# Kernel optimization log

Hardware: AMD Instinct MI355X
Metric: run time of the kernel (lower is better)

The kernel has to match this reference:

```python
import jax, jax.numpy as jnp
import numpy as np

LN_EPS = 1e-12


def setup_inputs() -> dict:
    key = jax.random.key(0)
    ks = jax.random.split(key, 5)
    E, H, I = 8, 768, 3072
    T = 2048  # tokens per expert (capacity-balanced)
    N = E * T
    return {
        "hidden_states": jax.random.normal(ks[0], (N, H), jnp.float32),
        "w1": jax.random.normal(ks[1], (E, H, I), jnp.float32) * (H ** -0.5),
        "b1": jax.random.normal(ks[2], (E, I), jnp.float32) * 0.02,
        "w2": jax.random.normal(ks[3], (E, I, H), jnp.float32) * (I ** -0.5),
        "b2": jax.random.normal(ks[4], (E, H), jnp.float32) * 0.02,
        "ln_gamma": jnp.ones((H,), jnp.float32),
        "ln_beta": jnp.zeros((H,), jnp.float32),
        "tokens_per_expert": T,
    }


def reference(hidden_states, w1, b1, w2, b2, ln_gamma, ln_beta, tokens_per_expert):
    E = w1.shape[0]
    N, H = hidden_states.shape
    # tokens are pre-sorted by expert; equal capacity per expert -> grouped GEMM
    x = hidden_states.reshape(E, tokens_per_expert, H)  # [E, T, H]
    # dense1 + exact GELU (BERT ACT2FN['gelu'])
    inter = jax.nn.gelu(jnp.einsum("eth,ehi->eti", x, w1) + b1[:, None, :],
                        approximate=False)  # [E, T, I]
    # dense2
    out = jnp.einsum("eti,eih->eth", inter, w2) + b2[:, None, :]  # [E, T, H]
    # dropout is identity in eval mode; residual + LayerNorm
    y = out.reshape(N, H) + hidden_states
    mean = jnp.mean(y, axis=-1, keepdims=True)
    var = jnp.mean(jnp.square(y - mean), axis=-1, keepdims=True)
    return (y - mean) * jax.lax.rsqrt(var + LN_EPS) * ln_gamma + ln_beta
```

## Files before the change

kernel.cpp:

```cpp
#include <hip/hip_runtime.h>
#include <hip/hip_bf16.h>
#include <math.h>

#define E_   8
#define H_   768
#define I_   3072
#define T_   2048
#define NTOK (E_ * T_)

typedef __attribute__((ext_vector_type(8))) short bf16x8;
typedef __attribute__((ext_vector_type(4))) float f32x4;

typedef __attribute__((address_space(3))) void lds_void;
typedef const __attribute__((address_space(1))) void gl_void;

__device__ __forceinline__ void gload16(const void* g, void* l) {
  __builtin_amdgcn_global_load_lds((gl_void*)g, (lds_void*)l, 16, 0, 0);
}

#define FENCE() asm volatile("" ::: "memory")
#define BAR()                         \
  do {                                \
    FENCE();                          \
    __builtin_amdgcn_s_barrier();     \
    FENCE();                          \
  } while (0)
#define VMWAIT(n) asm volatile("s_waitcnt vmcnt(" #n ")" ::: "memory")

#define MFMA16(a, b, c) __builtin_amdgcn_mfma_f32_16x16x32_bf16(a, b, c, 0, 0, 0)

__device__ __forceinline__ float gelu_fast(float v) {
  float inner = v * fmaf(v * v, 0.044715f, 1.0f);
  float e = __builtin_amdgcn_exp2f(inner * -2.3022082f);
  return v * __builtin_amdgcn_rcpf(1.0f + e);
}

#define CVT_BLOCKS 12288
#define WT_BLOCKS  4608

__global__ __launch_bounds__(256) void prep_kernel(
    const float* __restrict__ x, __hip_bfloat16* __restrict__ x_bf,
    const float* __restrict__ w1, __hip_bfloat16* __restrict__ w1t,
    const float* __restrict__ w2, __hip_bfloat16* __restrict__ w2t) {
  __shared__ __hip_bfloat16 tile[64][66];
  int b = blockIdx.x;

  if (b < CVT_BLOCKS) {
    int i = (b * 256 + threadIdx.x) * 4;
    float4 v = *(const float4*)(x + i);
    __align__(8) __hip_bfloat16 t[4];
    t[0] = __float2bfloat16(v.x);
    t[1] = __float2bfloat16(v.y);
    t[2] = __float2bfloat16(v.z);
    t[3] = __float2bfloat16(v.w);
    *(ushort4*)(x_bf + i) = *(const ushort4*)t;
    return;
  }

  const float* src;
  __hip_bfloat16* dst;
  int R, C, c0, r0;
  if (b < CVT_BLOCKS + WT_BLOCKS) {
    int t = b - CVT_BLOCKS;
    int e = t / 576, rem = t % 576;
    R = H_; C = I_;
    c0 = (rem % 48) * 64;
    r0 = (rem / 48) * 64;
    src = w1 + (size_t)e * R * C;
    dst = w1t + (size_t)e * R * C;
  } else {
    int t = b - (CVT_BLOCKS + WT_BLOCKS);
    int e = t / 576, rem = t % 576;
    R = I_; C = H_;
    c0 = (rem % 12) * 64;
    r0 = (rem / 12) * 64;
    src = w2 + (size_t)e * R * C;
    dst = w2t + (size_t)e * R * C;
  }

  int tx = threadIdx.x & 31;
  int ty = threadIdx.x >> 5;
#pragma unroll
  for (int r = ty; r < 64; r += 8) {
    float2 v = *(const float2*)&src[(size_t)(r0 + r) * C + c0 + 2 * tx];
    __hip_bfloat16 b0 = __float2bfloat16(v.x);
    __hip_bfloat16 b1 = __float2bfloat16(v.y);
    ushort2 w;
    w.x = *(const ushort*)&b0;
    w.y = *(const ushort*)&b1;
    *(ushort2*)&tile[r][2 * tx] = w;
  }
  __syncthreads();
#pragma unroll
  for (int rr = ty; rr < 64; rr += 8) {
    ushort2 v;
    v.x = *(const ushort*)&tile[2 * tx][rr];
    v.y = *(const ushort*)&tile[2 * tx + 1][rr];
    *(ushort2*)&dst[(size_t)(c0 + rr) * R + r0 + 2 * tx] = v;
  }
}

template <int K, int N, bool GELU>
__global__ __launch_bounds__(1024, 4) void gemm16w_kernel(
    const __hip_bfloat16* __restrict__ A,
    const __hip_bfloat16* __restrict__ B,
    const float* __restrict__ bias,
    __hip_bfloat16* __restrict__ out) {
  constexpr int BN = 256;
  constexpr int MT = T_ / 256;
  constexpr int NT = N / BN;
  constexpr int KT = K / 64;

  __shared__ __hip_bfloat16 sA[2][2][128][64];
  __shared__ __hip_bfloat16 sB[2][BN][64];

  int nwg = gridDim.x;
  int b0  = blockIdx.x;
  int bid = (b0 & 7) * (nwg >> 3) + (b0 >> 3);

  int e   = bid / (MT * NT);
  int rr_ = bid % (MT * NT);
  int bm  = rr_ / NT;
  int bn  = rr_ % NT;

  const __hip_bfloat16* Ae = A + (size_t)e * T_ * K + (size_t)bm * 256 * K;
  const __hip_bfloat16* Be = B + (size_t)e * N  * K + (size_t)bn * BN * K;

  int tid  = threadIdx.x;
  int lane = tid & 63;
  int wid  = tid >> 6;
  int wr   = wid >> 3;
  int wc   = wid & 7;
  int l15  = lane & 15;
  int l16h = lane >> 4;

  int lr0 = tid >> 3, c80 = tid & 7, cg0 = c80 ^ (lr0 & 7);
  int rA0 = ((lr0 >> 6) << 7) | (lr0 & 63);
  const size_t oA0 = (size_t)rA0 * K + cg0 * 8;
  const size_t HOFF = (size_t)64 * K;
  size_t oB[2];
  int    dB[2];
#pragma unroll
  for (int q = 0; q < 2; ++q) {
    int idx = q * 1024 + tid;
    int lr = idx >> 3, c8 = idx & 7;
    int cg = c8 ^ (lr & 7);
    oB[q] = (size_t)lr * K + cg * 8;
    dB[q] = lr * 64 + c8 * 8;
  }

  auto stageA = [&](int buf, int h, int kt) {
    const __hip_bfloat16* g = Ae + (size_t)kt * 64 + (size_t)h * HOFF;
    gload16(g + oA0, &sA[buf][h][lr0][c80 * 8]);
  };
  auto stageB = [&](int buf, int kt) {
    const __hip_bfloat16* g = Be + (size_t)kt * 64;
    __hip_bfloat16* l = &sB[buf][0][0];
    gload16(g + oB[0], l + dB[0]);
    gload16(g + oB[1], l + dB[1]);
  };

  int laBase = wr * 64 + l15;
  int lbBase = wc * 32 + l15;
  int s7   = l15 & 7;
  int cgr0 = ((0 | l16h) ^ s7) * 8;
  int cgr1 = ((4 | l16h) ^ s7) * 8;

  f32x4 acc[8][2] = {};
  bf16x8 af[4][2], bfv[2][2];

  stageA(0, 0, 0);
  stageB(0, 0);
  stageA(0, 1, 0);

  auto ktile = [&](int kt, int p, bool pf) {
    VMWAIT(1);
    BAR();
#pragma unroll
    for (int mf = 0; mf < 4; ++mf) {
      int la = laBase + mf * 16;
      af[mf][0] = *(const bf16x8*)&sA[p][0][la][cgr0];
      af[mf][1] = *(const bf16x8*)&sA[p][0][la][cgr1];
    }
#pragma unroll
    for (int nf = 0; nf < 2; ++nf) {
      int lb = lbBase + nf * 16;
      bfv[nf][0] = *(const bf16x8*)&sB[p][lb][cgr0];
      bfv[nf][1] = *(const bf16x8*)&sB[p][lb][cgr1];
    }
    if (pf) {
      stageA(p ^ 1, 0, kt + 1);
      stageB(p ^ 1, kt + 1);
    }
    __builtin_amdgcn_s_setprio(1);
#pragma unroll
    for (int mf = 0; mf < 4; ++mf)
#pragma unroll
      for (int nf = 0; nf < 2; ++nf) {
        acc[mf][nf] = MFMA16(af[mf][0], bfv[nf][0], acc[mf][nf]);
        acc[mf][nf] = MFMA16(af[mf][1], bfv[nf][1], acc[mf][nf]);
      }
    __builtin_amdgcn_s_setprio(0);
    if (pf) { VMWAIT(3); } else { VMWAIT(0); }
    BAR();
#pragma unroll
    for (int mf = 0; mf < 4; ++mf) {
      int la = laBase + mf * 16;
      af[mf][0] = *(const bf16x8*)&sA[p][1][la][cgr0];
      af[mf][1] = *(const bf16x8*)&sA[p][1][la][cgr1];
    }
    if (pf) stageA(p ^ 1, 1, kt + 1);
    __builtin_amdgcn_s_setprio(1);
#pragma unroll
    for (int mf = 0; mf < 4; ++mf)
#pragma unroll
      for (int nf = 0; nf < 2; ++nf) {
        acc[4 + mf][nf] = MFMA16(af[mf][0], bfv[nf][0], acc[4 + mf][nf]);
        acc[4 + mf][nf] = MFMA16(af[mf][1], bfv[nf][1], acc[4 + mf][nf]);
      }
    __builtin_amdgcn_s_setprio(0);
  };

  int p = 0;
  for (int kt = 0; kt < KT - 1; ++kt) {
    ktile(kt, p, true);
    p ^= 1;
  }
  ktile(KT - 1, p, false);

  const float* be = bias + (size_t)e * N + bn * BN;
  __hip_bfloat16* oe =
      out + (size_t)e * T_ * N + (size_t)(bm * 256) * N + bn * BN;
  int r4 = l16h * 4;
#pragma unroll
  for (int mi = 0; mi < 8; ++mi) {
    int mh = mi >> 2, mf = mi & 3;
    int rowb = wr * 128 + mh * 64 + mf * 16 + r4;
#pragma unroll
    for (int nf = 0; nf < 2; ++nf) {
      int cc   = wc * 32 + nf * 16 + l15;
      float bv = be[cc];
#pragma unroll
      for (int r = 0; r < 4; ++r) {
        float v = acc[mi][nf][r] + bv;
        if (GELU) v = gelu_fast(v);
        oe[(size_t)(rowb + r) * N + cc] = __float2bfloat16(v);
      }
    }
  }
}

template <int K, int N, bool GELU>
__global__ __launch_bounds__(768, 3) void gemm12w_kernel(
    const __hip_bfloat16* __restrict__ A,
    const __hip_bfloat16* __restrict__ B,
    const float* __restrict__ bias,
    __hip_bfloat16* __restrict__ out) {
  constexpr int BN = 192;
  constexpr int MT = T_ / 256;
  constexpr int NT = N / BN;
  constexpr int KT = K / 64;

  __shared__ __hip_bfloat16 sA[2][2][128][64];
  __shared__ __hip_bfloat16 sB[2][BN][64];

  int nwg = gridDim.x;
  int b0  = blockIdx.x;
  int bid = (b0 & 7) * (nwg >> 3) + (b0 >> 3);

  int e   = bid / (MT * NT);
  int rr_ = bid % (MT * NT);
  int bm  = rr_ / NT;
  int bn  = rr_ % NT;

  const __hip_bfloat16* Ae = A + (size_t)e * T_ * K + (size_t)bm * 256 * K;
  const __hip_bfloat16* Be = B + (size_t)e * N  * K + (size_t)bn * BN * K;

  int tid  = threadIdx.x;
  int lane = tid & 63;
  int wid  = tid >> 6;
  int wr   = wid / 6;
  int wc   = wid % 6;
  int l15  = lane & 15;
  int l16h = lane >> 4;
  bool isX = (tid < 512);

  int i0 = tid, i1 = 512 + tid;
  int lr0 = i0 >> 3, c80 = i0 & 7, cg0 = c80 ^ (lr0 & 7);
  int lr1 = i1 >> 3, c81 = i1 & 7, cg1 = c81 ^ (lr1 & 7);
  int rA0 = ((lr0 >> 6) << 7) | (lr0 & 63);
  int rA1 = ((lr1 >> 6) << 7) | (lr1 & 63);
  const size_t oA0 = (size_t)rA0 * K + cg0 * 8;
  const size_t oA1 = (size_t)rA1 * K + cg1 * 8;
  const size_t HOFF = (size_t)64 * K;
  size_t oB[2];
  int    dB[2];
#pragma unroll
  for (int q = 0; q < 2; ++q) {
    int idx = q * 768 + tid;
    int lr = idx >> 3, c8 = idx & 7;
    int cg = c8 ^ (lr & 7);
    oB[q] = (size_t)lr * K + cg * 8;
    dB[q] = lr * 64 + c8 * 8;
  }

  auto stageA = [&](int buf, int h, int kt) {
    if (isX) {
      const __hip_bfloat16* g = Ae + (size_t)kt * 64 + (size_t)h * HOFF;
      gload16(g + oA0, &sA[buf][h][lr0][c80 * 8]);
      gload16(g + oA1, &sA[buf][h][lr1][c81 * 8]);
    }
  };
  auto stageB = [&](int buf, int kt) {
    const __hip_bfloat16* g = Be + (size_t)kt * 64;
    __hip_bfloat16* l = &sB[buf][0][0];
    gload16(g + oB[0], l + dB[0]);
    gload16(g + oB[1], l + dB[1]);
  };

  int laBase = wr * 64 + l15;
  int lbBase = wc * 32 + l15;
  int s7   = l15 & 7;
  int cgr0 = ((0 | l16h) ^ s7) * 8;
  int cgr1 = ((4 | l16h) ^ s7) * 8;

  f32x4 acc[8][2] = {};
  bf16x8 af[4][2], bfv[2][2];

  stageA(0, 0, 0);
  stageB(0, 0);
  stageA(0, 1, 0);

  auto ktile = [&](int kt, int p, bool pf) {
    if (isX) { VMWAIT(2); } else { VMWAIT(0); }
    BAR();
#pragma unroll
    for (int mf = 0; mf < 4; ++mf) {
      int la = laBase + mf * 16;
      af[mf][0] = *(const bf16x8*)&sA[p][0][la][cgr0];
      af[mf][1] = *(const bf16x8*)&sA[p][0][la][cgr1];
    }
#pragma unroll
    for (int nf = 0; nf < 2; ++nf) {
      int lb = lbBase + nf * 16;
      bfv[nf][0] = *(const bf16x8*)&sB[p][lb][cgr0];
      bfv[nf][1] = *(const bf16x8*)&sB[p][lb][cgr1];
    }
    if (pf) {
      stageA(p ^ 1, 0, kt + 1);
      stageB(p ^ 1, kt + 1);
    }
    __builtin_amdgcn_s_setprio(1);
#pragma unroll
    for (int mf = 0; mf < 4; ++mf)
#pragma unroll
      for (int nf = 0; nf < 2; ++nf) {
        acc[mf][nf] = MFMA16(af[mf][0], bfv[nf][0], acc[mf][nf]);
        acc[mf][nf] = MFMA16(af[mf][1], bfv[nf][1], acc[mf][nf]);
      }
    __builtin_amdgcn_s_setprio(0);
    if (pf) {
      if (isX) { VMWAIT(4); }
    } else {
      if (isX) { VMWAIT(0); }
    }
    BAR();
#pragma unroll
    for (int mf = 0; mf < 4; ++mf) {
      int la = laBase + mf * 16;
      af[mf][0] = *(const bf16x8*)&sA[p][1][la][cgr0];
      af[mf][1] = *(const bf16x8*)&sA[p][1][la][cgr1];
    }
    if (pf) stageA(p ^ 1, 1, kt + 1);
    __builtin_amdgcn_s_setprio(1);
#pragma unroll
    for (int mf = 0; mf < 4; ++mf)
#pragma unroll
      for (int nf = 0; nf < 2; ++nf) {
        acc[4 + mf][nf] = MFMA16(af[mf][0], bfv[nf][0], acc[4 + mf][nf]);
        acc[4 + mf][nf] = MFMA16(af[mf][1], bfv[nf][1], acc[4 + mf][nf]);
      }
    __builtin_amdgcn_s_setprio(0);
  };

  int p = 0;
  for (int kt = 0; kt < KT - 1; ++kt) {
    ktile(kt, p, true);
    p ^= 1;
  }
  ktile(KT - 1, p, false);

  const float* be = bias + (size_t)e * N + bn * BN;
  __hip_bfloat16* oe =
      out + (size_t)e * T_ * N + (size_t)(bm * 256) * N + bn * BN;
  int r4 = l16h * 4;
#pragma unroll
  for (int mi = 0; mi < 8; ++mi) {
    int mh = mi >> 2, mf = mi & 3;
    int rowb = wr * 128 + mh * 64 + mf * 16 + r4;
#pragma unroll
    for (int nf = 0; nf < 2; ++nf) {
      int cc   = wc * 32 + nf * 16 + l15;
      float bv = be[cc];
#pragma unroll
      for (int r = 0; r < 4; ++r) {
        float v = acc[mi][nf][r] + bv;
        if (GELU) v = gelu_fast(v);
        oe[(size_t)(rowb + r) * N + cc] = __float2bfloat16(v);
      }
    }
  }
}

__global__ __launch_bounds__(384) void ln_kernel(
    const __hip_bfloat16* __restrict__ yraw,
    const __hip_bfloat16* __restrict__ xbf,
    const float* __restrict__ gamma, const float* __restrict__ beta,
    float* __restrict__ out) {
  int row  = blockIdx.x;
  int tid  = threadIdx.x;
  int lane = tid & 63, wid = tid >> 6;
  int c    = tid * 2;
  const __hip_bfloat16* yr = yraw + (size_t)row * H_;
  const __hip_bfloat16* xr = xbf + (size_t)row * H_;

  ushort2 ya = *(const ushort2*)&yr[c];
  ushort2 xa = *(const ushort2*)&xr[c];
  __hip_bfloat16 t;
  float v0, v1;
  *(ushort*)&t = ya.x; v0 = __bfloat162float(t);
  *(ushort*)&t = xa.x; v0 += __bfloat162float(t);
  *(ushort*)&t = ya.y; v1 = __bfloat162float(t);
  *(ushort*)&t = xa.y; v1 += __bfloat162float(t);

  float s = v0 + v1, s2 = v0 * v0 + v1 * v1;
#pragma unroll
  for (int o = 32; o > 0; o >>= 1) {
    s  += __shfl_down(s, o);
    s2 += __shfl_down(s2, o);
  }
  __shared__ float ls[6], ls2[6];
  if (lane == 0) { ls[wid] = s; ls2[wid] = s2; }
  __syncthreads();
  float tot  = ls[0] + ls[1] + ls[2] + ls[3] + ls[4] + ls[5];
  float tot2 = ls2[0] + ls2[1] + ls2[2] + ls2[3] + ls2[4] + ls2[5];
  float mean = tot * (1.0f / 768.0f);
  float var  = tot2 * (1.0f / 768.0f) - mean * mean;
  float inv  = rsqrtf(var + 1e-12f);
  float2 g = *(const float2*)&gamma[c];
  float2 b = *(const float2*)&beta[c];
  float2 o2;
  o2.x = (v0 - mean) * inv * g.x + b.x;
  o2.y = (v1 - mean) * inv * g.y + b.y;
  *(float2*)&out[(size_t)row * H_ + c] = o2;
}

extern "C" void kernel_launch(void* const* d_in, const int* in_sizes, int n_in,
                              void* d_out, int out_size, void* d_ws,
                              size_t ws_size, hipStream_t stream) {
  const float* x     = (const float*)d_in[0];
  const float* w1    = (const float*)d_in[1];
  const float* b1    = (const float*)d_in[2];
  const float* w2    = (const float*)d_in[3];
  const float* b2    = (const float*)d_in[4];
  const float* gamma = (const float*)d_in[5];
  const float* beta  = (const float*)d_in[6];
  float* out = (float*)d_out;

  char* ws = (char*)d_ws;
  __hip_bfloat16* w1t   = (__hip_bfloat16*)(ws);
  __hip_bfloat16* w2t   = (__hip_bfloat16*)(ws + 37748736);
  __hip_bfloat16* x_bf  = (__hip_bfloat16*)(ws + 75497472);
  __hip_bfloat16* inter = (__hip_bfloat16*)(ws + 100663296);
  __hip_bfloat16* yraw  = (__hip_bfloat16*)(ws);

  prep_kernel<<<CVT_BLOCKS + 2 * WT_BLOCKS, 256, 0, stream>>>(
      x, x_bf, w1, w1t, w2, w2t);
  gemm16w_kernel<H_, I_, true>
      <<<E_ * (T_ / 256) * (I_ / 256), 1024, 0, stream>>>(x_bf, w1t, b1, inter);
  gemm12w_kernel<I_, H_, false>
      <<<E_ * (T_ / 256) * (H_ / 192), 768, 0, stream>>>(inter, w2t, b2, yraw);
  ln_kernel<<<NTOK, 384, 0, stream>>>(yraw, x_bf, gamma, beta, out);
}
```

Baseline: 255.6 us.

## Use 8-wave blocks with larger per-wave tiles in first GEMM

Replaces the 16-wave 1024-thread GEMM1 kernel with a templated 8-wave 512-thread version. Each wave now covers 64 columns instead of 32, each thread issues twice as many async global-to-LDS loads, and the vmcnt waits are adjusted to match. The larger per-wave tile raises register reuse of A fragments and reduces barrier participants. The cost is higher register pressure (launch bounds 512,2) and fewer waves available to hide latency.

```diff
diff --git a/kernel.cpp b/kernel.cpp
--- a/kernel.cpp
+++ b/kernel.cpp
@@ -100,16 +100,18 @@
   }
 }
 
-template <int K, int N, bool GELU>
-__global__ __launch_bounds__(1024, 4) void gemm16w_kernel(
+template <int K, int N, int BN, bool GELU>
+__global__ __launch_bounds__(512, 2) void gemm2p_kernel(
     const __hip_bfloat16* __restrict__ A,
     const __hip_bfloat16* __restrict__ B,
     const float* __restrict__ bias,
     __hip_bfloat16* __restrict__ out) {
-  constexpr int BN = 256;
   constexpr int MT = T_ / 256;
   constexpr int NT = N / BN;
   constexpr int KT = K / 64;
+  constexpr int NF = BN / 64;
+  constexpr int WCW = BN / 4;
+  constexpr int BPASS = BN / 64;
 
   __shared__ __hip_bfloat16 sA[2][2][128][64];
   __shared__ __hip_bfloat16 sB[2][BN][64];
@@ -129,20 +131,24 @@
   int tid  = threadIdx.x;
   int lane = tid & 63;
   int wid  = tid >> 6;
-  int wr   = wid >> 3;
-  int wc   = wid & 7;
+  int wr   = wid >> 2;
+  int wc   = wid & 3;
   int l15  = lane & 15;
   int l16h = lane >> 4;
 
-  int lr0 = tid >> 3, c80 = tid & 7, cg0 = c80 ^ (lr0 & 7);
+  int i0 = tid, i1 = 512 + tid;
+  int lr0 = i0 >> 3, c80 = i0 & 7, cg0 = c80 ^ (lr0 & 7);
+  int lr1 = i1 >> 3, c81 = i1 & 7, cg1 = c81 ^ (lr1 & 7);
   int rA0 = ((lr0 >> 6) << 7) | (lr0 & 63);
+  int rA1 = ((lr1 >> 6) << 7) | (lr1 & 63);
   const size_t oA0 = (size_t)rA0 * K + cg0 * 8;
+  const size_t oA1 = (size_t)rA1 * K + cg1 * 8;
   const size_t HOFF = (size_t)64 * K;
-  size_t oB[2];
-  int    dB[2];
-#pragma unroll
-  for (int q = 0; q < 2; ++q) {
-    int idx = q * 1024 + tid;
+  size_t oB[BPASS];
+  int    dB[BPASS];
+#pragma unroll
+  for (int q = 0; q < BPASS; ++q) {
+    int idx = q * 512 + tid;
     int lr = idx >> 3, c8 = idx & 7;
     int cg = c8 ^ (lr & 7);
     oB[q] = (size_t)lr * K + cg * 8;
@@ -152,29 +158,30 @@
   auto stageA = [&](int buf, int h, int kt) {
     const __hip_bfloat16* g = Ae + (size_t)kt * 64 + (size_t)h * HOFF;
     gload16(g + oA0, &sA[buf][h][lr0][c80 * 8]);
+    gload16(g + oA1, &sA[buf][h][lr1][c81 * 8]);
   };
   auto stageB = [&](int buf, int kt) {
     const __hip_bfloat16* g = Be + (size_t)kt * 64;
     __hip_bfloat16* l = &sB[buf][0][0];
-    gload16(g + oB[0], l + dB[0]);
-    gload16(g + oB[1], l + dB[1]);
+#pragma unroll
+    for (int q = 0; q < BPASS; ++q) gload16(g + oB[q], l + dB[q]);
   };
 
   int laBase = wr * 64 + l15;
-  int lbBase = wc * 32 + l15;
+  int lbBase = wc * WCW + l15;
   int s7   = l15 & 7;
   int cgr0 = ((0 | l16h) ^ s7) * 8;
   int cgr1 = ((4 | l16h) ^ s7) * 8;
 
-  f32x4 acc[8][2] = {};
-  bf16x8 af[4][2], bfv[2][2];
+  f32x4 acc[8][NF] = {};
+  bf16x8 af[4][2], bfv[NF][2];
 
   stageA(0, 0, 0);
   stageB(0, 0);
   stageA(0, 1, 0);
 
   auto ktile = [&](int kt, int p, bool pf) {
-    VMWAIT(1);
+    VMWAIT(2);
     BAR();
 #pragma unroll
     for (int mf = 0; mf < 4; ++mf) {
@@ -183,7 +190,7 @@
       af[mf][1] = *(const bf16x8*)&sA[p][0][la][cgr1];
     }
 #pragma unroll
-    for (int nf = 0; nf < 2; ++nf) {
+    for (int nf = 0; nf < NF; ++nf) {
       int lb = lbBase + nf * 16;
       bfv[nf][0] = *(const bf16x8*)&sB[p][lb][cgr0];
       bfv[nf][1] = *(const bf16x8*)&sB[p][lb][cgr1];
@@ -196,12 +203,16 @@
 #pragma unroll
     for (int mf = 0; mf < 4; ++mf)
 #pragma unroll
-      for (int nf = 0; nf < 2; ++nf) {
+      for (int nf = 0; nf < NF; ++nf) {
         acc[mf][nf] = MFMA16(af[mf][0], bfv[nf][0], acc[mf][nf]);
         acc[mf][nf] = MFMA16(af[mf][1], bfv[nf][1], acc[mf][nf]);
       }
     __builtin_amdgcn_s_setprio(0);
-    if (pf) { VMWAIT(3); } else { VMWAIT(0); }
+    if (pf) {
+      if constexpr (BN == 256) { VMWAIT(6); } else { VMWAIT(5); }
+    } else {
+      VMWAIT(0);
+    }
     BAR();
 #pragma unroll
     for (int mf = 0; mf < 4; ++mf) {
@@ -214,7 +225,7 @@
 #pragma unroll
     for (int mf = 0; mf < 4; ++mf)
 #pragma unroll
-      for (int nf = 0; nf < 2; ++nf) {
+      for (int nf = 0; nf < NF; ++nf) {
         acc[4 + mf][nf] = MFMA16(af[mf][0], bfv[nf][0], acc[4 + mf][nf]);
         acc[4 + mf][nf] = MFMA16(af[mf][1], bfv[nf][1], acc[4 + mf][nf]);
       }
@@ -237,8 +248,8 @@
     int mh = mi >> 2, mf = mi & 3;
     int rowb = wr * 128 + mh * 64 + mf * 16 + r4;
 #pragma unroll
-    for (int nf = 0; nf < 2; ++nf) {
-      int cc   = wc * 32 + nf * 16 + l15;
+    for (int nf = 0; nf < NF; ++nf) {
+      int cc   = wc * WCW + nf * 16 + l15;
       float bv = be[cc];
 #pragma unroll
       for (int r = 0; r < 4; ++r) {
@@ -476,8 +487,8 @@
 
   prep_kernel<<<CVT_BLOCKS + 2 * WT_BLOCKS, 256, 0, stream>>>(
       x, x_bf, w1, w1t, w2, w2t);
-  gemm16w_kernel<H_, I_, true>
-      <<<E_ * (T_ / 256) * (I_ / 256), 1024, 0, stream>>>(x_bf, w1t, b1, inter);
+  gemm2p_kernel<H_, I_, 256, true>
+      <<<E_ * (T_ / 256) * (I_ / 256), 512, 0, stream>>>(x_bf, w1t, b1, inter);
   gemm12w_kernel<I_, H_, false>
       <<<E_ * (T_ / 256) * (H_ / 192), 768, 0, stream>>>(inter, w2t, b2, yraw);
   ln_kernel<<<NTOK, 384, 0, stream>>>(yraw, x_bf, gamma, beta, out);
```

Result: faster. 239.1 us (-6.4%).
